# Kernel tuning notes

Measured on AMD Instinct MI355X. Metric: run time of the kernel, lower is better.

Reference implementation:

```python
import jax, jax.numpy as jnp
import numpy as np

B, C, H, W = 4, 256, 64, 64
CK = C // 8  # query/key channels per OUT_RATIO=8


def setup_inputs() -> dict:
    key = jax.random.key(0)
    ks = jax.random.split(key, 8)
    s_in = 1.0 / np.sqrt(C)
    return {
        "x": jax.random.normal(ks[0], (B, C, H, W), dtype=jnp.float32),
        "Wq": jax.random.uniform(ks[1], (CK, C), jnp.float32, -s_in, s_in),
        "bq": jax.random.uniform(ks[2], (CK,), jnp.float32, -s_in, s_in),
        "Wk": jax.random.uniform(ks[3], (CK, C), jnp.float32, -s_in, s_in),
        "bk": jax.random.uniform(ks[4], (CK,), jnp.float32, -s_in, s_in),
        "Wv": jax.random.uniform(ks[5], (C, C), jnp.float32, -s_in, s_in),
        "bv": jax.random.uniform(ks[6], (C,), jnp.float32, -s_in, s_in),
        "gamma": jnp.zeros((1,), dtype=jnp.float32),
    }


def reference(x, Wq, bq, Wk, bk, Wv, bv, gamma):
    b, c, h, w = x.shape
    n = h * w
    xf = x.reshape(b, c, n)  # [B, C, N]
    # 1x1 convs are channel matmuls
    q = jnp.einsum('oc,bcn->bno', Wq, xf) + bq  # [B, N, CK]
    k = jnp.einsum('oc,bcn->bon', Wk, xf) + bk[None, :, None]  # [B, CK, N]
    v = jnp.einsum('oc,bcn->bon', Wv, xf) + bv[None, :, None]  # [B, C, N]
    energy = jnp.einsum('bno,bom->bnm', q, k)  # [B, N, N], unscaled
    attn = jax.nn.softmax(energy, axis=-1)
    out = jnp.einsum('bcm,bnm->bcn', v, attn)  # [B, C, N]
    out = out.reshape(b, c, h, w)
    return gamma[0] * out + x
```

## Files before the change

### kernel.cpp

```cpp
#include <hip/hip_runtime.h>
#include <math.h>


#define BB 4
#define CC 256
#define NN 4096
#define CKK 32
#define LOG2E 1.44269504f

typedef __attribute__((ext_vector_type(4))) float f32x4;
typedef __attribute__((ext_vector_type(16))) float f32x16;
typedef __attribute__((ext_vector_type(8))) short short8;
typedef __attribute__((ext_vector_type(4))) short short4v;

static __device__ __forceinline__ ushort f2bf(float f) {
    union { float f; unsigned u; } v; v.f = f;
    unsigned r = v.u + 0x7FFFu + ((v.u >> 16) & 1u);
    return (ushort)(r >> 16);
}
static __device__ __forceinline__ float bf2f(ushort h) {
    union { unsigned u; float f; } v; v.u = ((unsigned)h) << 16;
    return v.f;
}
static __device__ __forceinline__ unsigned pack2(float lo, float hi) {
    unsigned r;
    asm("v_cvt_pk_bf16_f32 %0, %1, %2" : "=v"(r) : "v"(lo), "v"(hi));
    return r;
}
static __device__ __forceinline__ float exp2fast(float x) {
    return __builtin_amdgcn_exp2f(x);
}

__global__ __launch_bounds__(256) void pack_w_kernel(
    const float* __restrict__ Wq, const float* __restrict__ bq,
    const float* __restrict__ Wk, const float* __restrict__ bk,
    const float* __restrict__ Wv, const float* __restrict__ bv,
    ushort* __restrict__ Wb, float* __restrict__ bias)
{
    const int o = blockIdx.x;
    const int c = threadIdx.x;
    const float* src; float bsc;
    if (o < 32)      { src = Wq + o * CC;        bsc = bq[o]; }
    else if (o < 64) { src = Wk + (o - 32) * CC; bsc = bk[o - 32]; }
    else             { src = Wv + (o - 64) * CC; bsc = bv[o - 64]; }
    Wb[o * CC + c] = f2bf(src[c]);
    if (c == 0) bias[o] = bsc;
}

__global__ __launch_bounds__(256) void qkv_mfma_kernel(
    const ushort* __restrict__ Wb, const float* __restrict__ bias,
    const float* __restrict__ x,
    ushort* __restrict__ Q, ushort* __restrict__ Kt, ushort* __restrict__ V)
{
    const int b = blockIdx.y, n0 = blockIdx.x * 64;
    const int tid = threadIdx.x;
    const int w = tid >> 6, lane = tid & 63, l15 = lane & 15, q = lane >> 4;

    f32x4 acc[5][4];
    #pragma unroll
    for (int c5 = 0; c5 < 5; ++c5)
        #pragma unroll
        for (int nc = 0; nc < 4; ++nc) acc[c5][nc] = (f32x4)0.f;

    const float* xb = x + (size_t)b * CC * NN + n0;

    #pragma unroll
    for (int ks = 0; ks < 8; ++ks) {
        short8 af[5];
        #pragma unroll
        for (int c5 = 0; c5 < 5; ++c5)
            af[c5] = *(const short8*)&Wb[(w * 80 + c5 * 16 + l15) * CC + ks * 32 + q * 8];
        union { unsigned u[4]; short8 v; } bfu[4];
        #pragma unroll
        for (int nc = 0; nc < 4; ++nc) {
            const float* xp = xb + (size_t)(ks * 32 + q * 8) * NN + nc * 16 + l15;
            bfu[nc].u[0] = pack2(xp[0],          xp[(size_t)NN]);
            bfu[nc].u[1] = pack2(xp[2 * (size_t)NN], xp[3 * (size_t)NN]);
            bfu[nc].u[2] = pack2(xp[4 * (size_t)NN], xp[5 * (size_t)NN]);
            bfu[nc].u[3] = pack2(xp[6 * (size_t)NN], xp[7 * (size_t)NN]);
        }
        #pragma unroll
        for (int c5 = 0; c5 < 5; ++c5)
            #pragma unroll
            for (int nc = 0; nc < 4; ++nc)
                acc[c5][nc] = __builtin_amdgcn_mfma_f32_16x16x32_bf16(af[c5], bfu[nc].v, acc[c5][nc], 0, 0, 0);
    }

    #pragma unroll
    for (int c5 = 0; c5 < 5; ++c5) {
        const int o0 = w * 80 + c5 * 16;
        float bia[4];
        #pragma unroll
        for (int r = 0; r < 4; ++r) bia[r] = bias[o0 + q * 4 + r];
        if (o0 >= 64) {
            #pragma unroll
            for (int nc = 0; nc < 4; ++nc)
                #pragma unroll
                for (int r = 0; r < 4; ++r)
                    V[((size_t)b * CC + o0 - 64 + q * 4 + r) * NN + n0 + nc * 16 + l15] =
                        f2bf(acc[c5][nc][r] + bia[r]);
        } else {
            ushort* dst = (o0 < 32) ? Q : Kt;
            const float sc = (o0 < 32) ? LOG2E : 1.0f;
            const int oo = (o0 & 31) + q * 4;
            #pragma unroll
            for (int nc = 0; nc < 4; ++nc) {
                short4v h;
                #pragma unroll
                for (int r = 0; r < 4; ++r) h[r] = (short)f2bf((acc[c5][nc][r] + bia[r]) * sc);
                *(short4v*)&dst[((size_t)b * NN + n0 + nc * 16 + l15) * CKK + oo] = h;
            }
        }
    }
}

__global__ __launch_bounds__(256, 2) void attn_mfma_kernel(
    const ushort* __restrict__ Q, const ushort* __restrict__ K,
    const ushort* __restrict__ V,
    ushort* __restrict__ Op, float* __restrict__ Mp, float* __restrict__ Lp,
    int G, int NSEG)
{
    __shared__ __align__(16) ushort vs2[2][4][256][8];

    const int id = blockIdx.x;
    const int xcd = id & 7, ix = id >> 3;
    const int b = xcd >> 1;
    int g, row;
    if (G == 4) { g = ((xcd & 1) << 1) | (ix & 1); row = ix >> 1; }
    else        { g = xcd & 1;                     row = ix; }
    const int n0 = row * 128;

    const int tid = threadIdx.x;
    const int w = tid >> 6, lane = tid & 63;
    const int l31 = lane & 31, h2 = lane >> 5;
    const int n0w = n0 + w * 32;

    const size_t qrow = ((size_t)b * NN + n0w + l31) * CKK;
    short8 qB0 = *(const short8*)&Q[qrow + h2 * 8];
    short8 qB1 = *(const short8*)&Q[qrow + 16 + h2 * 8];

    f32x16 acc[8];
    #pragma unroll
    for (int cb = 0; cb < 8; ++cb) acc[cb] = (f32x16)0.f;
    float m_i = -3.0e38f, l_p = 0.f;

    const ushort* Kb = K + (size_t)b * NN * CKK;
    const size_t vgb = (size_t)b * CC * NN;
    const int m_start = g * NSEG;
    const int NT = NSEG / 32;

    const int srow = tid >> 2, sseg = tid & 3;
    const int kh2a = (sseg >> 1) << 1;
    const int sslot = (sseg & 1) << 2;

    short8 kA0 = *(const short8*)&Kb[(size_t)(m_start + l31) * CKK + h2 * 8];
    short8 kA1 = *(const short8*)&Kb[(size_t)(m_start + l31) * CKK + 16 + h2 * 8];
    union { short8 v; short4v h[2]; } vr[4];
    #pragma unroll
    for (int i = 0; i < 4; ++i)
        vr[i].v = *(const short8*)&V[vgb + (size_t)(srow + i * 64) * NN + m_start + sseg * 8];
    f32x16 s = __builtin_amdgcn_mfma_f32_32x32x16_bf16(kA0, qB0, (f32x16)0.f, 0, 0, 0);
    s = __builtin_amdgcn_mfma_f32_32x32x16_bf16(kA1, qB1, s, 0, 0, 0);
    const int mi1 = (NT > 1) ? m_start + 32 : m_start;
    kA0 = *(const short8*)&Kb[(size_t)(mi1 + l31) * CKK + h2 * 8];
    kA1 = *(const short8*)&Kb[(size_t)(mi1 + l31) * CKK + 16 + h2 * 8];
    #pragma unroll
    for (int i = 0; i < 4; ++i) {
        const int c = srow + i * 64;
        *(short4v*)&vs2[0][kh2a + 0][c][sslot] = vr[i].h[0];
        *(short4v*)&vs2[0][kh2a + 1][c][sslot] = vr[i].h[1];
    }
    #pragma unroll
    for (int i = 0; i < 4; ++i)
        vr[i].v = *(const short8*)&V[vgb + (size_t)(srow + i * 64) * NN + mi1 + sseg * 8];
    __syncthreads();

    int cur = 0;
    for (int mt = 0; mt < NT; ++mt) {
        const bool more = (mt + 1 < NT);
        const int mi2 = (mt + 2 < NT) ? m_start + (mt + 2) * 32 : m_start;

        f32x16 sn = __builtin_amdgcn_mfma_f32_32x32x16_bf16(kA0, qB0, (f32x16)0.f, 0, 0, 0);
        sn = __builtin_amdgcn_mfma_f32_32x32x16_bf16(kA1, qB1, sn, 0, 0, 0);
        kA0 = *(const short8*)&Kb[(size_t)(mi2 + l31) * CKK + h2 * 8];
        kA1 = *(const short8*)&Kb[(size_t)(mi2 + l31) * CKK + 16 + h2 * 8];

        float t0 = fmaxf(fmaxf(s[0],  s[1]),  s[2]);
        float t1 = fmaxf(fmaxf(s[3],  s[4]),  s[5]);
        float t2 = fmaxf(fmaxf(s[6],  s[7]),  s[8]);
        float t3 = fmaxf(fmaxf(s[9],  s[10]), s[11]);
        float t4 = fmaxf(fmaxf(s[12], s[13]), s[14]);
        float mx = fmaxf(fmaxf(fmaxf(t0, t1), t2), fmaxf(fmaxf(t3, t4), s[15]));
        mx = fmaxf(mx, __shfl_xor(mx, 32));
        const bool resc = mx > m_i + 8.f;
        const float mn = resc ? mx : m_i;
        const float al = resc ? exp2fast(m_i - mx) : 1.f;
        union { unsigned u[8]; short8 v[2]; } P;
        float sum0 = 0.f, sum1 = 0.f;
        #pragma unroll
        for (int g2 = 0; g2 < 8; ++g2) {
            const float plo = exp2fast(s[2 * g2]     - mn);
            const float phi = exp2fast(s[2 * g2 + 1] - mn);
            if (g2 & 1) sum1 += plo + phi; else sum0 += plo + phi;
            P.u[g2] = pack2(plo, phi);
        }
        l_p = l_p * al + (sum0 + sum1);
        m_i = mn;
        if (__any(resc)) {
            #pragma unroll
            for (int cb = 0; cb < 8; ++cb) acc[cb] *= al;
        }

        __builtin_amdgcn_s_setprio(1);
        #pragma unroll
        for (int cb = 0; cb < 8; ++cb) {
            const short8 A0 = *(const short8*)&vs2[cur][h2][cb * 32 + l31][0];
            const short8 A1 = *(const short8*)&vs2[cur][2 + h2][cb * 32 + l31][0];
            acc[cb] = __builtin_amdgcn_mfma_f32_32x32x16_bf16(A0, P.v[0], acc[cb], 0, 0, 0);
            acc[cb] = __builtin_amdgcn_mfma_f32_32x32x16_bf16(A1, P.v[1], acc[cb], 0, 0, 0);
        }
        __builtin_amdgcn_s_setprio(0);

        if (more) {
            #pragma unroll
            for (int i = 0; i < 4; ++i) {
                const int c = srow + i * 64;
                *(short4v*)&vs2[cur ^ 1][kh2a + 0][c][sslot] = vr[i].h[0];
                *(short4v*)&vs2[cur ^ 1][kh2a + 1][c][sslot] = vr[i].h[1];
            }
            __syncthreads();
            #pragma unroll
            for (int i = 0; i < 4; ++i)
                vr[i].v = *(const short8*)&V[vgb + (size_t)(srow + i * 64) * NN + mi2 + sseg * 8];
        }
        s = sn; cur ^= 1;
    }

    float l = l_p + __shfl_xor(l_p, 32);
    const float linv = 1.f / l;
    if (h2 == 0) {
        const size_t idx = (size_t)(g * BB + b) * NN + n0w + l31;
        Mp[idx] = m_i;
        Lp[idx] = l;
    }
    ushort* ob = Op + (size_t)(g * BB + b) * CC * NN;
    #pragma unroll
    for (int cb = 0; cb < 8; ++cb)
        #pragma unroll
        for (int r = 0; r < 16; ++r) {
            const int c = cb * 32 + (r & 3) + 8 * (r >> 2) + 4 * h2;
            ob[(size_t)c * NN + n0w + l31] = f2bf(acc[cb][r] * linv);
        }
}

template<int G>
__global__ __launch_bounds__(256) void combine_kernel(
    const ushort* __restrict__ Op, const float* __restrict__ Mp,
    const float* __restrict__ Lp, const float* __restrict__ x,
    const float* __restrict__ gamma, float* __restrict__ out)
{
    const int gid = blockIdx.x * 256 + threadIdx.x;
    const int grp   = gid & (NN / 8 - 1);
    const int rowid = gid >> 9;
    const int b = rowid >> 8;
    const int c = rowid & (CC - 1);
    const int n0 = grp * 8;

    f32x4 mp[G][2], lp[G][2];
    #pragma unroll
    for (int g = 0; g < G; ++g) {
        const size_t base = (size_t)(g * BB + b) * NN + n0;
        mp[g][0] = *(const f32x4*)&Mp[base];
        mp[g][1] = *(const f32x4*)&Mp[base + 4];
        lp[g][0] = *(const f32x4*)&Lp[base];
        lp[g][1] = *(const f32x4*)&Lp[base + 4];
    }
    float wgt[G][8];
    #pragma unroll
    for (int h = 0; h < 2; ++h) {
        #pragma unroll
        for (int j = 0; j < 4; ++j) {
            float M = -3.0e38f;
            #pragma unroll
            for (int g = 0; g < G; ++g) M = fmaxf(M, mp[g][h][j]);
            float ws = 0.f;
            #pragma unroll
            for (int g = 0; g < G; ++g) {
                const float wv = lp[g][h][j] * exp2fast(mp[g][h][j] - M);
                wgt[g][h * 4 + j] = wv;
                ws += wv;
            }
            const float inv = 1.f / ws;
            #pragma unroll
            for (int g = 0; g < G; ++g) wgt[g][h * 4 + j] *= inv;
        }
    }

    short8 opv[G];
    #pragma unroll
    for (int g = 0; g < G; ++g)
        opv[g] = *(const short8*)&Op[((size_t)(g * BB + b) * CC + c) * NN + n0];

    const size_t xbase = ((size_t)b * CC + c) * NN + n0;
    const f32x4 x0 = *(const f32x4*)&x[xbase];
    const f32x4 x1 = *(const f32x4*)&x[xbase + 4];
    const float gm = gamma[0];

    f32x4 o0, o1;
    #pragma unroll
    for (int j = 0; j < 4; ++j) {
        float a = 0.f, bsum = 0.f;
        #pragma unroll
        for (int g = 0; g < G; ++g) {
            a    += wgt[g][j]     * bf2f((ushort)opv[g][j]);
            bsum += wgt[g][4 + j] * bf2f((ushort)opv[g][4 + j]);
        }
        o0[j] = gm * a + x0[j];
        o1[j] = gm * bsum + x1[j];
    }
    *(f32x4*)&out[xbase]     = o0;
    *(f32x4*)&out[xbase + 4] = o1;
}

extern "C" void kernel_launch(void* const* d_in, const int* in_sizes, int n_in,
                              void* d_out, int out_size, void* d_ws, size_t ws_size,
                              hipStream_t stream) {
    const float* x     = (const float*)d_in[0];
    const float* Wq    = (const float*)d_in[1];
    const float* bq    = (const float*)d_in[2];
    const float* Wk    = (const float*)d_in[3];
    const float* bk    = (const float*)d_in[4];
    const float* Wv    = (const float*)d_in[5];
    const float* bv    = (const float*)d_in[6];
    const float* gamma = (const float*)d_in[7];
    float* out = (float*)d_out;

    char* p = (char*)d_ws;
    ushort* Wb   = (ushort*)(p);
    float*  bias = (float*) (p + 163840);
    ushort* Qb   = (ushort*)(p + 165120);
    ushort* Kb   = (ushort*)(p + 1213696);
    ushort* Vc   = (ushort*)(p + 2262272);
    float*  Mpb  = (float*) (p + 10650880);
    float*  Lpb  = (float*) (p + 10913024);
    ushort* Opb  = (ushort*)(p + 11175168);
    const int G = (ws_size >= (size_t)44729600) ? 4 : 2;

    pack_w_kernel<<<dim3(320), 256, 0, stream>>>(Wq, bq, Wk, bk, Wv, bv, Wb, bias);
    qkv_mfma_kernel<<<dim3(NN / 64, BB), 256, 0, stream>>>(Wb, bias, x, Qb, Kb, Vc);
    attn_mfma_kernel<<<dim3(128 * G), 256, 0, stream>>>(Qb, Kb, Vc, Opb, Mpb, Lpb, G, NN / G);
    const int cblocks = BB * CC * (NN / 8) / 256;
    if (G == 4)
        combine_kernel<4><<<dim3(cblocks), 256, 0, stream>>>(Opb, Mpb, Lpb, x, gamma, out);
    else
        combine_kernel<2><<<dim3(cblocks), 256, 0, stream>>>(Opb, Mpb, Lpb, x, gamma, out);
}
```

Baseline: 89.34 us.

## Store V pre-tiled in MFMA operand layout and read directly from global

The QKV projection now writes V in a tiled layout that matches the attention kernel's MFMA A-operand fragments, 32 keys by 256 channels per tile. The attention kernel drops the double-buffered LDS staging of V and its per-tile __syncthreads, loading each fragment straight from global/L2 with 16-byte reads. This removes the LDS write/read traffic and block barriers, but exposes global load latency inside the PV MFMA loop with no explicit prefetch. The QKV kernel's V stores also become scattered 2-byte writes.

```diff
diff --git a/kernel.cpp b/kernel.cpp
--- a/kernel.cpp
+++ b/kernel.cpp
@@ -50,7 +50,7 @@
 __global__ __launch_bounds__(256) void qkv_mfma_kernel(
     const ushort* __restrict__ Wb, const float* __restrict__ bias,
     const float* __restrict__ x,
-    ushort* __restrict__ Q, ushort* __restrict__ Kt, ushort* __restrict__ V)
+    ushort* __restrict__ Q, ushort* __restrict__ Kt, ushort* __restrict__ Vg)
 {
     const int b = blockIdx.y, n0 = blockIdx.x * 64;
     const int tid = threadIdx.x;
@@ -74,7 +74,7 @@
         #pragma unroll
         for (int nc = 0; nc < 4; ++nc) {
             const float* xp = xb + (size_t)(ks * 32 + q * 8) * NN + nc * 16 + l15;
-            bfu[nc].u[0] = pack2(xp[0],          xp[(size_t)NN]);
+            bfu[nc].u[0] = pack2(xp[0],              xp[(size_t)NN]);
             bfu[nc].u[1] = pack2(xp[2 * (size_t)NN], xp[3 * (size_t)NN]);
             bfu[nc].u[2] = pack2(xp[4 * (size_t)NN], xp[5 * (size_t)NN]);
             bfu[nc].u[3] = pack2(xp[6 * (size_t)NN], xp[7 * (size_t)NN]);
@@ -86,6 +86,9 @@
                 acc[c5][nc] = __builtin_amdgcn_mfma_f32_16x16x32_bf16(af[c5], bfu[nc].v, acc[c5][nc], 0, 0, 0);
     }
 
+    const int kh2b = (l15 >> 2) & 1;
+    const int jj   = (l15 & 3) + ((l15 >> 3) << 2);
+
     #pragma unroll
     for (int c5 = 0; c5 < 5; ++c5) {
         const int o0 = w * 80 + c5 * 16;
@@ -94,11 +97,16 @@
         for (int r = 0; r < 4; ++r) bia[r] = bias[o0 + q * 4 + r];
         if (o0 >= 64) {
             #pragma unroll
-            for (int nc = 0; nc < 4; ++nc)
+            for (int nc = 0; nc < 4; ++nc) {
+                const size_t tbase =
+                    ((size_t)b * (NN / 32) + (n0 >> 5) + (nc >> 1)) * 8192
+                    + (size_t)(((nc & 1) << 1) + kh2b) * 2048 + jj;
                 #pragma unroll
-                for (int r = 0; r < 4; ++r)
-                    V[((size_t)b * CC + o0 - 64 + q * 4 + r) * NN + n0 + nc * 16 + l15] =
-                        f2bf(acc[c5][nc][r] + bia[r]);
+                for (int r = 0; r < 4; ++r) {
+                    const int c = o0 - 64 + q * 4 + r;
+                    Vg[tbase + c * 8] = f2bf(acc[c5][nc][r] + bia[r]);
+                }
+            }
         } else {
             ushort* dst = (o0 < 32) ? Q : Kt;
             const float sc = (o0 < 32) ? LOG2E : 1.0f;
@@ -116,12 +124,10 @@
 
 __global__ __launch_bounds__(256, 2) void attn_mfma_kernel(
     const ushort* __restrict__ Q, const ushort* __restrict__ K,
-    const ushort* __restrict__ V,
+    const ushort* __restrict__ Vg,
     ushort* __restrict__ Op, float* __restrict__ Mp, float* __restrict__ Lp,
     int G, int NSEG)
 {
-    __shared__ __align__(16) ushort vs2[2][4][256][8];
-
     const int id = blockIdx.x;
     const int xcd = id & 7, ix = id >> 3;
     const int b = xcd >> 1;
@@ -145,39 +151,22 @@
     float m_i = -3.0e38f, l_p = 0.f;
 
     const ushort* Kb = K + (size_t)b * NN * CKK;
-    const size_t vgb = (size_t)b * CC * NN;
+    const ushort* Vb = Vg + (size_t)b * (NN / 32) * 8192;
     const int m_start = g * NSEG;
     const int NT = NSEG / 32;
 
-    const int srow = tid >> 2, sseg = tid & 3;
-    const int kh2a = (sseg >> 1) << 1;
-    const int sslot = (sseg & 1) << 2;
+    const size_t voff0 = (size_t)h2 * 2048 + (size_t)l31 * 8;
+    const size_t voff1 = (size_t)(2 + h2) * 2048 + (size_t)l31 * 8;
 
     short8 kA0 = *(const short8*)&Kb[(size_t)(m_start + l31) * CKK + h2 * 8];
     short8 kA1 = *(const short8*)&Kb[(size_t)(m_start + l31) * CKK + 16 + h2 * 8];
-    union { short8 v; short4v h[2]; } vr[4];
-    #pragma unroll
-    for (int i = 0; i < 4; ++i)
-        vr[i].v = *(const short8*)&V[vgb + (size_t)(srow + i * 64) * NN + m_start + sseg * 8];
     f32x16 s = __builtin_amdgcn_mfma_f32_32x32x16_bf16(kA0, qB0, (f32x16)0.f, 0, 0, 0);
     s = __builtin_amdgcn_mfma_f32_32x32x16_bf16(kA1, qB1, s, 0, 0, 0);
     const int mi1 = (NT > 1) ? m_start + 32 : m_start;
     kA0 = *(const short8*)&Kb[(size_t)(mi1 + l31) * CKK + h2 * 8];
     kA1 = *(const short8*)&Kb[(size_t)(mi1 + l31) * CKK + 16 + h2 * 8];
-    #pragma unroll
-    for (int i = 0; i < 4; ++i) {
-        const int c = srow + i * 64;
-        *(short4v*)&vs2[0][kh2a + 0][c][sslot] = vr[i].h[0];
-        *(short4v*)&vs2[0][kh2a + 1][c][sslot] = vr[i].h[1];
-    }
-    #pragma unroll
-    for (int i = 0; i < 4; ++i)
-        vr[i].v = *(const short8*)&V[vgb + (size_t)(srow + i * 64) * NN + mi1 + sseg * 8];
-    __syncthreads();
-
-    int cur = 0;
+
     for (int mt = 0; mt < NT; ++mt) {
-        const bool more = (mt + 1 < NT);
         const int mi2 = (mt + 2 < NT) ? m_start + (mt + 2) * 32 : m_start;
 
         f32x16 sn = __builtin_amdgcn_mfma_f32_32x32x16_bf16(kA0, qB0, (f32x16)0.f, 0, 0, 0);
@@ -211,29 +200,18 @@
             for (int cb = 0; cb < 8; ++cb) acc[cb] *= al;
         }
 
+        const ushort* Vt = Vb + (size_t)(m_start / 32 + mt) * 8192;
         __builtin_amdgcn_s_setprio(1);
         #pragma unroll
         for (int cb = 0; cb < 8; ++cb) {
-            const short8 A0 = *(const short8*)&vs2[cur][h2][cb * 32 + l31][0];
-            const short8 A1 = *(const short8*)&vs2[cur][2 + h2][cb * 32 + l31][0];
+            const short8 A0 = *(const short8*)&Vt[voff0 + cb * 256];
+            const short8 A1 = *(const short8*)&Vt[voff1 + cb * 256];
             acc[cb] = __builtin_amdgcn_mfma_f32_32x32x16_bf16(A0, P.v[0], acc[cb], 0, 0, 0);
             acc[cb] = __builtin_amdgcn_mfma_f32_32x32x16_bf16(A1, P.v[1], acc[cb], 0, 0, 0);
         }
         __builtin_amdgcn_s_setprio(0);
 
-        if (more) {
-            #pragma unroll
-            for (int i = 0; i < 4; ++i) {
-                const int c = srow + i * 64;
-                *(short4v*)&vs2[cur ^ 1][kh2a + 0][c][sslot] = vr[i].h[0];
-                *(short4v*)&vs2[cur ^ 1][kh2a + 1][c][sslot] = vr[i].h[1];
-            }
-            __syncthreads();
-            #pragma unroll
-            for (int i = 0; i < 4; ++i)
-                vr[i].v = *(const short8*)&V[vgb + (size_t)(srow + i * 64) * NN + mi2 + sseg * 8];
-        }
-        s = sn; cur ^= 1;
+        s = sn;
     }
 
     float l = l_p + __shfl_xor(l_p, 32);
```

New measurement: 129.5 us. 44.9% more time.
